# Performance work log

Measured on AMD Instinct MI355X. Metric: run time of the kernel, lower is better.

Reference implementation:

```python
import jax, jax.numpy as jnp
import numpy as np

S, H, A = 8192, 4096, 1024

def setup_inputs() -> dict:
    key = jax.random.key(0)
    ks = jax.random.split(key, 8)
    return {
        "encoder_outputs": jax.random.normal(ks[0], (S, H), jnp.float32),
        "hidden": jax.random.normal(ks[1], (H,), jnp.float32),
        "U_w": jax.random.normal(ks[2], (A, H), jnp.float32) * (1.0 / np.sqrt(H)),
        "U_b": jax.random.normal(ks[3], (A,), jnp.float32) * 0.01,
        "W_w": jax.random.normal(ks[4], (A, H), jnp.float32) * (1.0 / np.sqrt(H)),
        "W_b": jax.random.normal(ks[5], (A,), jnp.float32) * 0.01,
        "V_w": jax.random.normal(ks[6], (1, A), jnp.float32) * (1.0 / np.sqrt(A)),
        "V_b": jax.random.normal(ks[7], (1,), jnp.float32) * 0.01,
    }

def reference(encoder_outputs, hidden, U_w, U_b, W_w, W_b, V_w, V_b):
    # Bahdanau additive attention ('add' mode).
    W_hidden = hidden @ W_w.T + W_b                      # [A]
    U_encode = encoder_outputs @ U_w.T + U_b             # [S, A]
    poly_tanh = jnp.tanh(U_encode + W_hidden)            # [S, A]
    scores = poly_tanh @ V_w.T + V_b                     # [S, 1]
    attn = jax.nn.softmax(scores, axis=0)                # softmax over sequence
    context = attn.T @ encoder_outputs                   # [1, H]
    return context[None]                                 # [1, 1, H] (matches torch bmm)
```

## Files before the change

kernel.cpp:

```cpp
#include <hip/hip_runtime.h>

typedef __attribute__((ext_vector_type(8))) short short8;
typedef __attribute__((ext_vector_type(4))) float f32x4;

#define S_DIM 8192
#define H_DIM 4096
#define A_DIM 1024

__device__ __forceinline__ short f2bf(float x) {
  unsigned u = __float_as_uint(x);
  u += 0x7fffu + ((u >> 16) & 1u);
  return (short)(u >> 16);
}

__device__ __forceinline__ float bf2f(short b) {
  return __uint_as_float(((unsigned)(unsigned short)b) << 16);
}

__device__ __forceinline__ void gload16(const void* g, void* l) {
  __builtin_amdgcn_global_load_lds(
      (const __attribute__((address_space(1))) void*)g,
      (__attribute__((address_space(3))) void*)l, 16, 0, 0);
}

__global__ __launch_bounds__(256) void comb_kernel(const float* __restrict__ hidden,
                                                   const float* __restrict__ Ww,
                                                   const float* __restrict__ Wb,
                                                   const float* __restrict__ Ub,
                                                   float* __restrict__ comb) {
  const int wave = threadIdx.x >> 6;
  const int lane = threadIdx.x & 63;
  const int a = blockIdx.x * 4 + wave;
  const float* row = Ww + (size_t)a * H_DIM;
  float acc = 0.f;
  for (int k = lane * 4; k < H_DIM; k += 64 * 4) {
    float4 w = *(const float4*)(row + k);
    float4 h = *(const float4*)(hidden + k);
    acc += w.x * h.x + w.y * h.y + w.z * h.z + w.w * h.w;
  }
  #pragma unroll
  for (int mk = 1; mk < 64; mk <<= 1) acc += __shfl_xor(acc, mk);
  if (lane == 0) comb[a] = acc + Wb[a] + Ub[a];
}

__global__ __launch_bounds__(256) void cvt_kernel(const float* __restrict__ src,
                                                  unsigned short* __restrict__ dst,
                                                  int n8) {
  const int stride = gridDim.x * blockDim.x;
  for (int i = blockIdx.x * blockDim.x + threadIdx.x; i < n8; i += stride) {
    float4 a = ((const float4*)src)[(size_t)i * 2];
    float4 b = ((const float4*)src)[(size_t)i * 2 + 1];
    short8 o;
    o[0] = f2bf(a.x); o[1] = f2bf(a.y); o[2] = f2bf(a.z); o[3] = f2bf(a.w);
    o[4] = f2bf(b.x); o[5] = f2bf(b.y); o[6] = f2bf(b.z); o[7] = f2bf(b.w);
    ((short8*)dst)[i] = o;
  }
}

__global__ __launch_bounds__(256) void gemm_score_t64_kernel(
    const unsigned short* __restrict__ A,
    const unsigned short* __restrict__ B,
    const float* __restrict__ comb,
    const float* __restrict__ Vw,
    float* __restrict__ scores) {
  __shared__ __align__(16) unsigned short sA[128 * 64];
  __shared__ __align__(16) unsigned short sB[64 * 64];

  const int tid  = threadIdx.x;
  const int lane = tid & 63;
  const int wave = tid >> 6;
  const int wm = wave >> 1, wn = wave & 1;
  const int m0 = blockIdx.x * 128;
  const int n0 = blockIdx.y * 64;

  const int scol  = (lane & 7) * 8;
  const unsigned short* ga = A + (size_t)(m0 + wave * 32 + (lane >> 3)) * H_DIM + scol;
  const unsigned short* gb = B + (size_t)(n0 + wave * 16 + (lane >> 3)) * H_DIM + scol;

  #define STAGE(kt) do {                                                     \
    const unsigned short* pa_ = ga + (size_t)(kt) * 64;                      \
    const unsigned short* pb_ = gb + (size_t)(kt) * 64;                      \
    _Pragma("unroll")                                                        \
    for (int i_ = 0; i_ < 4; ++i_)                                           \
      gload16(pa_ + (size_t)i_ * 8 * H_DIM, &sA[(wave * 4 + i_) * 512]);     \
    _Pragma("unroll")                                                        \
    for (int i_ = 0; i_ < 2; ++i_)                                           \
      gload16(pb_ + (size_t)i_ * 8 * H_DIM, &sB[(wave * 2 + i_) * 512]);     \
  } while (0)

  f32x4 acc[4][2];
  const f32x4 zero = {0.f, 0.f, 0.f, 0.f};
  #pragma unroll
  for (int i = 0; i < 4; ++i)
    #pragma unroll
    for (int j = 0; j < 2; ++j) acc[i][j] = zero;

  STAGE(0);

  const int NK = H_DIM / 64;
  for (int kt = 0; kt < NK; ++kt) {
    __syncthreads();

    short8 af[2][4], bfr[2][2];
    #pragma unroll
    for (int ks = 0; ks < 2; ++ks) {
      #pragma unroll
      for (int i = 0; i < 4; ++i)
        af[ks][i] = *(const short8*)&sA[(wm * 64 + i * 16 + (lane & 15)) * 64 + ks * 32 + (lane >> 4) * 8];
      #pragma unroll
      for (int j = 0; j < 2; ++j)
        bfr[ks][j] = *(const short8*)&sB[(wn * 32 + j * 16 + (lane & 15)) * 64 + ks * 32 + (lane >> 4) * 8];
    }
    __syncthreads();

    if (kt + 1 < NK) STAGE(kt + 1);

    #pragma unroll
    for (int ks = 0; ks < 2; ++ks)
      #pragma unroll
      for (int i = 0; i < 4; ++i)
        #pragma unroll
        for (int j = 0; j < 2; ++j)
          acc[i][j] = __builtin_amdgcn_mfma_f32_16x16x32_bf16(af[ks][i], bfr[ks][j], acc[i][j], 0, 0, 0);
  }
  #undef STAGE

  float vwv[2], cbv[2];
  #pragma unroll
  for (int j = 0; j < 2; ++j) {
    const int col = n0 + wn * 32 + j * 16 + (lane & 15);
    vwv[j] = Vw[col];
    cbv[j] = comb[col];
  }
  #pragma unroll
  for (int i = 0; i < 4; ++i) {
    #pragma unroll
    for (int r = 0; r < 4; ++r) {
      float s = vwv[0] * tanhf(acc[i][0][r] + cbv[0])
              + vwv[1] * tanhf(acc[i][1][r] + cbv[1]);
      s += __shfl_xor(s, 1);
      s += __shfl_xor(s, 2);
      s += __shfl_xor(s, 4);
      s += __shfl_xor(s, 8);
      if ((lane & 15) == 0) {
        const int grow = m0 + wm * 64 + i * 16 + (lane >> 4) * 4 + r;
        atomicAdd(&scores[grow], s);
      }
    }
  }
}

__global__ __launch_bounds__(1024) void softmax_kernel(const float* __restrict__ scores,
                                                       float* __restrict__ attn) {
  __shared__ float redm[16];
  __shared__ float reds[16];
  const int tid = threadIdx.x;
  const int lane = tid & 63, wid = tid >> 6;
  float v[8];
  float m = -3.0e38f;
  #pragma unroll
  for (int i = 0; i < 8; ++i) { v[i] = scores[i * 1024 + tid]; m = fmaxf(m, v[i]); }
  #pragma unroll
  for (int mk = 1; mk < 64; mk <<= 1) m = fmaxf(m, __shfl_xor(m, mk));
  if (lane == 0) redm[wid] = m;
  __syncthreads();
  float M = redm[0];
  #pragma unroll
  for (int j = 1; j < 16; ++j) M = fmaxf(M, redm[j]);
  float e[8]; float s = 0.f;
  #pragma unroll
  for (int i = 0; i < 8; ++i) { e[i] = __expf(v[i] - M); s += e[i]; }
  #pragma unroll
  for (int mk = 1; mk < 64; mk <<= 1) s += __shfl_xor(s, mk);
  if (lane == 0) reds[wid] = s;
  __syncthreads();
  float T = 0.f;
  #pragma unroll
  for (int j = 0; j < 16; ++j) T += reds[j];
  const float inv = 1.f / T;
  #pragma unroll
  for (int i = 0; i < 8; ++i) attn[i * 1024 + tid] = e[i] * inv;
}

__global__ __launch_bounds__(256) void context_bf_kernel(const unsigned short* __restrict__ Ebf,
                                                         const float* __restrict__ attn,
                                                         float* __restrict__ partial) {
  const int h0 = (blockIdx.x * 256 + threadIdx.x) * 8;
  const int s0 = blockIdx.y * 64;
  float acc[8] = {0.f, 0.f, 0.f, 0.f, 0.f, 0.f, 0.f, 0.f};
  for (int s = s0; s < s0 + 64; ++s) {
    const float w = attn[s];
    short8 e = *(const short8*)(Ebf + (size_t)s * H_DIM + h0);
    #pragma unroll
    for (int j = 0; j < 8; ++j) acc[j] += w * bf2f(e[j]);
  }
  float* p = partial + (size_t)blockIdx.y * H_DIM + h0;
  #pragma unroll
  for (int j = 0; j < 8; ++j) p[j] = acc[j];
}

__global__ __launch_bounds__(256) void context_reduce_kernel(const float* __restrict__ partial,
                                                             float* __restrict__ out) {
  const int h = blockIdx.x * 256 + threadIdx.x;
  float acc = 0.f;
  #pragma unroll 8
  for (int y = 0; y < 128; ++y) acc += partial[(size_t)y * H_DIM + h];
  out[h] = acc;
}


#define LDSW 40
__global__ __launch_bounds__(256) void gemm_score_kernel(const float* __restrict__ E,
                                                         const float* __restrict__ Uw,
                                                         const float* __restrict__ comb,
                                                         const float* __restrict__ Vw,
                                                         float* __restrict__ scores) {
  __shared__ __align__(16) short sA[128 * LDSW];
  __shared__ __align__(16) short sB[128 * LDSW];
  const int tid  = threadIdx.x;
  const int lane = tid & 63;
  const int wave = tid >> 6;
  const int wm = wave >> 1, wn = wave & 1;
  const int m0 = blockIdx.x * 128;
  const int n0 = blockIdx.y * 128;
  const int sr = tid >> 1;
  const int sh = tid & 1;
  const float* gA = E  + (size_t)(m0 + sr) * H_DIM + sh * 16;
  const float* gB = Uw + (size_t)(n0 + sr) * H_DIM + sh * 16;
  alignas(16) float fa[16], fb[16];
  #pragma unroll
  for (int j = 0; j < 4; ++j) {
    *(float4*)&fa[j * 4] = *(const float4*)(gA + j * 4);
    *(float4*)&fb[j * 4] = *(const float4*)(gB + j * 4);
  }
  f32x4 acc[4][4];
  const f32x4 zero = {0.f, 0.f, 0.f, 0.f};
  #pragma unroll
  for (int i = 0; i < 4; ++i)
    #pragma unroll
    for (int j = 0; j < 4; ++j) acc[i][j] = zero;
  short* wA = &sA[sr * LDSW + sh * 16];
  short* wB = &sB[sr * LDSW + sh * 16];
  const int NK = H_DIM / 32;
  for (int kt = 0; kt < NK; ++kt) {
    short8 ca0, ca1, cb0, cb1;
    #pragma unroll
    for (int j = 0; j < 8; ++j) {
      ca0[j] = f2bf(fa[j]);     ca1[j] = f2bf(fa[8 + j]);
      cb0[j] = f2bf(fb[j]);     cb1[j] = f2bf(fb[8 + j]);
    }
    __syncthreads();
    *(short8*)(wA)     = ca0;
    *(short8*)(wA + 8) = ca1;
    *(short8*)(wB)     = cb0;
    *(short8*)(wB + 8) = cb1;
    __syncthreads();
    if (kt + 1 < NK) {
      const float* pA = gA + (kt + 1) * 32;
      const float* pB = gB + (kt + 1) * 32;
      #pragma unroll
      for (int j = 0; j < 4; ++j) {
        *(float4*)&fa[j * 4] = *(const float4*)(pA + j * 4);
        *(float4*)&fb[j * 4] = *(const float4*)(pB + j * 4);
      }
    }
    short8 af[4], bfr[4];
    #pragma unroll
    for (int i = 0; i < 4; ++i)
      af[i] = *(const short8*)&sA[(wm * 64 + i * 16 + (lane & 15)) * LDSW + (lane >> 4) * 8];
    #pragma unroll
    for (int j = 0; j < 4; ++j)
      bfr[j] = *(const short8*)&sB[(wn * 64 + j * 16 + (lane & 15)) * LDSW + (lane >> 4) * 8];
    #pragma unroll
    for (int i = 0; i < 4; ++i)
      #pragma unroll
      for (int j = 0; j < 4; ++j)
        acc[i][j] = __builtin_amdgcn_mfma_f32_16x16x32_bf16(af[i], bfr[j], acc[i][j], 0, 0, 0);
  }
  float vwv[4], cbv[4];
  #pragma unroll
  for (int j = 0; j < 4; ++j) {
    const int col = n0 + wn * 64 + j * 16 + (lane & 15);
    vwv[j] = Vw[col];
    cbv[j] = comb[col];
  }
  #pragma unroll
  for (int i = 0; i < 4; ++i) {
    #pragma unroll
    for (int r = 0; r < 4; ++r) {
      float s = 0.f;
      #pragma unroll
      for (int j = 0; j < 4; ++j)
        s += vwv[j] * tanhf(acc[i][j][r] + cbv[j]);
      s += __shfl_xor(s, 1);
      s += __shfl_xor(s, 2);
      s += __shfl_xor(s, 4);
      s += __shfl_xor(s, 8);
      if ((lane & 15) == 0) {
        const int grow = m0 + wm * 64 + i * 16 + (lane >> 4) * 4 + r;
        atomicAdd(&scores[grow], s);
      }
    }
  }
}

__global__ __launch_bounds__(256) void context_kernel(const float* __restrict__ E,
                                                      const float* __restrict__ attn,
                                                      float* __restrict__ out) {
  const int h  = blockIdx.x * 256 + threadIdx.x;
  const int s0 = blockIdx.y * 256;
  float acc = 0.f;
  #pragma unroll 4
  for (int s = s0; s < s0 + 256; ++s)
    acc += attn[s] * E[(size_t)s * H_DIM + h];
  atomicAdd(&out[h], acc);
}


extern "C" void kernel_launch(void* const* d_in, const int* in_sizes, int n_in,
                              void* d_out, int out_size, void* d_ws, size_t ws_size,
                              hipStream_t stream) {
  const float* E   = (const float*)d_in[0];
  const float* hid = (const float*)d_in[1];
  const float* Uw  = (const float*)d_in[2];
  const float* Ub  = (const float*)d_in[3];
  const float* Ww  = (const float*)d_in[4];
  const float* Wb  = (const float*)d_in[5];
  const float* Vw  = (const float*)d_in[6];

  float* out    = (float*)d_out;
  float* ws     = (float*)d_ws;
  float* comb   = ws;
  float* scores = ws + 1024;
  float* attn   = ws + 1024 + 8192;
  float* ctxp   = ws + 17408;
  const size_t CTXP = (size_t)128 * H_DIM;

  unsigned short* Ebf  = (unsigned short*)(ws + 17408 + CTXP);
  unsigned short* Uwbf = Ebf + (size_t)S_DIM * H_DIM;
  const size_t NEED = ((size_t)17408 + CTXP) * 4
                    + ((size_t)S_DIM + A_DIM) * H_DIM * 2;

  hipMemsetAsync(scores, 0, S_DIM * sizeof(float), stream);

  comb_kernel<<<A_DIM / 4, 256, 0, stream>>>(hid, Ww, Wb, Ub, comb);

  if (ws_size >= NEED) {
    cvt_kernel<<<2048, 256, 0, stream>>>(E, Ebf, (int)((size_t)S_DIM * H_DIM / 8));
    cvt_kernel<<<512, 256, 0, stream>>>(Uw, Uwbf, (int)((size_t)A_DIM * H_DIM / 8));

    gemm_score_t64_kernel<<<dim3(S_DIM / 128, A_DIM / 64), 256, 0, stream>>>(
        Ebf, Uwbf, comb, Vw, scores);

    softmax_kernel<<<1, 1024, 0, stream>>>(scores, attn);

    context_bf_kernel<<<dim3(H_DIM / 2048, S_DIM / 64), 256, 0, stream>>>(Ebf, attn, ctxp);
    context_reduce_kernel<<<H_DIM / 256, 256, 0, stream>>>(ctxp, out);
  } else {
    hipMemsetAsync(out, 0, (size_t)out_size * sizeof(float), stream);
    gemm_score_kernel<<<dim3(S_DIM / 128, A_DIM / 128), 256, 0, stream>>>(E, Uw, comb, Vw, scores);
    softmax_kernel<<<1, 1024, 0, stream>>>(scores, attn);
    context_kernel<<<dim3(H_DIM / 256, 32), 256, 0, stream>>>(E, attn, out);
  }
}
```

Baseline: 182.6 us.

## Rework score GEMM with larger 256x128 tiles, triple-buffered LDS and XOR swizzle

Replaces the 128x64 single-buffered score GEMM with a 512-thread kernel using 256x128 block tiles, a 3-stage LDS ring with asynchronous global-to-LDS loads issued two tiles ahead, and one barrier per K step. LDS columns are XOR-swizzled to cut bank conflicts on fragment reads, and setprio is raised around the MFMA bursts. Each wave now computes a 64x64 tile, which doubles register accumulators and raises LDS use to about 144KB per block, so occupancy may be limited.

```diff
diff --git a/kernel.cpp b/kernel.cpp
--- a/kernel.cpp
+++ b/kernel.cpp
@@ -57,78 +57,92 @@
   }
 }
 
-__global__ __launch_bounds__(256) void gemm_score_t64_kernel(
+__global__ __launch_bounds__(512, 2) void gemm_score_8p_kernel(
     const unsigned short* __restrict__ A,
     const unsigned short* __restrict__ B,
     const float* __restrict__ comb,
     const float* __restrict__ Vw,
     float* __restrict__ scores) {
-  __shared__ __align__(16) unsigned short sA[128 * 64];
-  __shared__ __align__(16) unsigned short sB[64 * 64];
+  __shared__ __align__(16) unsigned short sA[3][256 * 64];
+  __shared__ __align__(16) unsigned short sB[3][128 * 64];
 
   const int tid  = threadIdx.x;
   const int lane = tid & 63;
   const int wave = tid >> 6;
-  const int wm = wave >> 1, wn = wave & 1;
-  const int m0 = blockIdx.x * 128;
-  const int n0 = blockIdx.y * 64;
-
-  const int scol  = (lane & 7) * 8;
-  const unsigned short* ga = A + (size_t)(m0 + wave * 32 + (lane >> 3)) * H_DIM + scol;
-  const unsigned short* gb = B + (size_t)(n0 + wave * 16 + (lane >> 3)) * H_DIM + scol;
-
-  #define STAGE(kt) do {                                                     \
-    const unsigned short* pa_ = ga + (size_t)(kt) * 64;                      \
-    const unsigned short* pb_ = gb + (size_t)(kt) * 64;                      \
-    _Pragma("unroll")                                                        \
-    for (int i_ = 0; i_ < 4; ++i_)                                           \
-      gload16(pa_ + (size_t)i_ * 8 * H_DIM, &sA[(wave * 4 + i_) * 512]);     \
-    _Pragma("unroll")                                                        \
-    for (int i_ = 0; i_ < 2; ++i_)                                           \
-      gload16(pb_ + (size_t)i_ * 8 * H_DIM, &sB[(wave * 2 + i_) * 512]);     \
+  const int wm = wave >> 1;
+  const int wn = wave & 1;
+  const int m0 = blockIdx.x * 256;
+  const int n0 = blockIdx.y * 128;
+
+  const int permEl = (((lane & 7) ^ (lane >> 3)) * 8);
+  const unsigned short* gA = A + (size_t)(m0 + wave * 32 + (lane >> 3)) * H_DIM + permEl;
+  const unsigned short* gB = B + (size_t)(n0 + wave * 16 + (lane >> 3)) * H_DIM + permEl;
+
+  #define STAGE(kt, bf) do {                                                  \
+    const unsigned short* pa_ = gA + (size_t)(kt) * 64;                       \
+    const unsigned short* pb_ = gB + (size_t)(kt) * 64;                       \
+    _Pragma("unroll")                                                         \
+    for (int l_ = 0; l_ < 4; ++l_)                                            \
+      gload16(pa_ + (size_t)l_ * 8 * H_DIM, &sA[bf][(wave * 4 + l_) * 512]);  \
+    _Pragma("unroll")                                                         \
+    for (int l_ = 0; l_ < 2; ++l_)                                            \
+      gload16(pb_ + (size_t)l_ * 8 * H_DIM, &sB[bf][(wave * 2 + l_) * 512]);  \
   } while (0)
 
-  f32x4 acc[4][2];
+  const int rA  = lane & 15;
+  const int grp = lane >> 4;
+  const int lx  = lane & 7;
+
+  f32x4 acc[4][4];
   const f32x4 zero = {0.f, 0.f, 0.f, 0.f};
   #pragma unroll
   for (int i = 0; i < 4; ++i)
     #pragma unroll
-    for (int j = 0; j < 2; ++j) acc[i][j] = zero;
-
-  STAGE(0);
-
-  const int NK = H_DIM / 64;
-  for (int kt = 0; kt < NK; ++kt) {
-    __syncthreads();
-
-    short8 af[2][4], bfr[2][2];
+    for (int j = 0; j < 4; ++j) acc[i][j] = zero;
+
+  STAGE(0, 0);
+  STAGE(1, 1);
+  asm volatile("s_waitcnt vmcnt(6)");
+  __builtin_amdgcn_s_barrier();
+  __builtin_amdgcn_sched_barrier(0);
+
+  const int NT = H_DIM / 64;
+  for (int t = 0; t < NT; ++t) {
+    const int cur = t % 3;
+    if (t + 2 < NT) STAGE(t + 2, (t + 2) % 3);
+
+    const unsigned short* a_ = sA[cur];
+    const unsigned short* b_ = sB[cur];
     #pragma unroll
     for (int ks = 0; ks < 2; ++ks) {
+      short8 af[4], bfr[4];
       #pragma unroll
       for (int i = 0; i < 4; ++i)
-        af[ks][i] = *(const short8*)&sA[(wm * 64 + i * 16 + (lane & 15)) * 64 + ks * 32 + (lane >> 4) * 8];
-      #pragma unroll
-      for (int j = 0; j < 2; ++j)
-        bfr[ks][j] = *(const short8*)&sB[(wn * 32 + j * 16 + (lane & 15)) * 64 + ks * 32 + (lane >> 4) * 8];
-    }
-    __syncthreads();
-
-    if (kt + 1 < NK) STAGE(kt + 1);
-
-    #pragma unroll
-    for (int ks = 0; ks < 2; ++ks)
+        af[i] = *(const short8*)&a_[(wm * 64 + i * 16 + rA) * 64 + (((ks * 4 + grp) ^ lx) * 8)];
+      #pragma unroll
+      for (int j = 0; j < 4; ++j)
+        bfr[j] = *(const short8*)&b_[(wn * 64 + j * 16 + rA) * 64 + (((ks * 4 + grp) ^ lx) * 8)];
+      __builtin_amdgcn_s_setprio(1);
       #pragma unroll
       for (int i = 0; i < 4; ++i)
         #pragma unroll
-        for (int j = 0; j < 2; ++j)
-          acc[i][j] = __builtin_amdgcn_mfma_f32_16x16x32_bf16(af[ks][i], bfr[ks][j], acc[i][j], 0, 0, 0);
+        for (int j = 0; j < 4; ++j)
+          acc[i][j] = __builtin_amdgcn_mfma_f32_16x16x32_bf16(af[i], bfr[j], acc[i][j], 0, 0, 0);
+      __builtin_amdgcn_s_setprio(0);
+    }
+
+    __builtin_amdgcn_sched_barrier(0);
+    if (t < NT - 2) asm volatile("s_waitcnt vmcnt(6)");
+    else            asm volatile("s_waitcnt vmcnt(0)");
+    __builtin_amdgcn_s_barrier();
+    __builtin_amdgcn_sched_barrier(0);
   }
   #undef STAGE
 
-  float vwv[2], cbv[2];
-  #pragma unroll
-  for (int j = 0; j < 2; ++j) {
-    const int col = n0 + wn * 32 + j * 16 + (lane & 15);
+  float vwv[4], cbv[4];
+  #pragma unroll
+  for (int j = 0; j < 4; ++j) {
+    const int col = n0 + wn * 64 + j * 16 + rA;
     vwv[j] = Vw[col];
     cbv[j] = comb[col];
   }
@@ -136,14 +150,16 @@
   for (int i = 0; i < 4; ++i) {
     #pragma unroll
     for (int r = 0; r < 4; ++r) {
-      float s = vwv[0] * tanhf(acc[i][0][r] + cbv[0])
-              + vwv[1] * tanhf(acc[i][1][r] + cbv[1]);
+      float s = 0.f;
+      #pragma unroll
+      for (int j = 0; j < 4; ++j)
+        s += vwv[j] * tanhf(acc[i][j][r] + cbv[j]);
       s += __shfl_xor(s, 1);
       s += __shfl_xor(s, 2);
       s += __shfl_xor(s, 4);
       s += __shfl_xor(s, 8);
-      if ((lane & 15) == 0) {
-        const int grow = m0 + wm * 64 + i * 16 + (lane >> 4) * 4 + r;
+      if (rA == 0) {
+        const int grow = m0 + wm * 64 + i * 16 + grp * 4 + r;
         atomicAdd(&scores[grow], s);
       }
     }
@@ -349,7 +365,7 @@
     cvt_kernel<<<2048, 256, 0, stream>>>(E, Ebf, (int)((size_t)S_DIM * H_DIM / 8));
     cvt_kernel<<<512, 256, 0, stream>>>(Uw, Uwbf, (int)((size_t)A_DIM * H_DIM / 8));
 
-    gemm_score_t64_kernel<<<dim3(S_DIM / 128, A_DIM / 64), 256, 0, stream>>>(
+    gemm_score_8p_kernel<<<dim3(S_DIM / 256, A_DIM / 128), 512, 0, stream>>>(
         Ebf, Uwbf, comb, Vw, scores);
 
     softmax_kernel<<<1, 1024, 0, stream>>>(scores, attn);
```

After: 164.2 us. -10.0%, faster.

## Use two-wave 64x64 per-wave tiles in score GEMM and fast tanh

Applied to the files above, without the earlier changes.

Restructures the score GEMM from four waves each computing a 64x32 sub-tile to two waves each computing a 64x64 sub-tile of the same 128x64 block tile. Each wave reads all of the B tile from shared memory and issues more global-to-LDS loads per stage. The aim is more MFMA work per LDS fragment load. It also swaps tanhf for an exp-and-divide approximation in the epilogue. The trade-off is fewer waves per block and more accumulator registers per wave, which may reduce latency hiding, plus slightly lower tanh accuracy.

```diff
diff --git a/kernel.cpp b/kernel.cpp
--- a/kernel.cpp
+++ b/kernel.cpp
@@ -15,6 +15,12 @@
 
 __device__ __forceinline__ float bf2f(short b) {
   return __uint_as_float(((unsigned)(unsigned short)b) << 16);
+}
+
+__device__ __forceinline__ float fast_tanh(float x) {
+  float e = __expf(-2.f * fabsf(x));
+  float r = __fdividef(1.f - e, 1.f + e);
+  return copysignf(r, x);
 }
 
 __device__ __forceinline__ void gload16(const void* g, void* l) {
@@ -57,7 +63,7 @@
   }
 }
 
-__global__ __launch_bounds__(256) void gemm_score_t64_kernel(
+__global__ __launch_bounds__(128) void gemm_score_f_kernel(
     const unsigned short* __restrict__ A,
     const unsigned short* __restrict__ B,
     const float* __restrict__ comb,
@@ -69,31 +75,30 @@
   const int tid  = threadIdx.x;
   const int lane = tid & 63;
   const int wave = tid >> 6;
-  const int wm = wave >> 1, wn = wave & 1;
   const int m0 = blockIdx.x * 128;
   const int n0 = blockIdx.y * 64;
 
-  const int scol  = (lane & 7) * 8;
-  const unsigned short* ga = A + (size_t)(m0 + wave * 32 + (lane >> 3)) * H_DIM + scol;
-  const unsigned short* gb = B + (size_t)(n0 + wave * 16 + (lane >> 3)) * H_DIM + scol;
-
-  #define STAGE(kt) do {                                                     \
-    const unsigned short* pa_ = ga + (size_t)(kt) * 64;                      \
-    const unsigned short* pb_ = gb + (size_t)(kt) * 64;                      \
-    _Pragma("unroll")                                                        \
-    for (int i_ = 0; i_ < 4; ++i_)                                           \
-      gload16(pa_ + (size_t)i_ * 8 * H_DIM, &sA[(wave * 4 + i_) * 512]);     \
-    _Pragma("unroll")                                                        \
-    for (int i_ = 0; i_ < 2; ++i_)                                           \
-      gload16(pb_ + (size_t)i_ * 8 * H_DIM, &sB[(wave * 2 + i_) * 512]);     \
+  const int scol = (lane & 7) * 8;
+  const unsigned short* ga = A + (size_t)(m0 + wave * 64 + (lane >> 3)) * H_DIM + scol;
+  const unsigned short* gb = B + (size_t)(n0 + wave * 32 + (lane >> 3)) * H_DIM + scol;
+
+  #define STAGE(kt) do {                                                      \
+    const unsigned short* pa_ = ga + (size_t)(kt) * 64;                       \
+    const unsigned short* pb_ = gb + (size_t)(kt) * 64;                       \
+    _Pragma("unroll")                                                         \
+    for (int i_ = 0; i_ < 8; ++i_)                                            \
+      gload16(pa_ + (size_t)i_ * 8 * H_DIM, &sA[(wave * 64 + i_ * 8) * 64]);  \
+    _Pragma("unroll")                                                         \
+    for (int i_ = 0; i_ < 4; ++i_)                                            \
+      gload16(pb_ + (size_t)i_ * 8 * H_DIM, &sB[(wave * 32 + i_ * 8) * 64]);  \
   } while (0)
 
-  f32x4 acc[4][2];
+  f32x4 acc[4][4];
   const f32x4 zero = {0.f, 0.f, 0.f, 0.f};
   #pragma unroll
   for (int i = 0; i < 4; ++i)
     #pragma unroll
-    for (int j = 0; j < 2; ++j) acc[i][j] = zero;
+    for (int j = 0; j < 4; ++j) acc[i][j] = zero;
 
   STAGE(0);
 
@@ -101,15 +106,15 @@
   for (int kt = 0; kt < NK; ++kt) {
     __syncthreads();
 
-    short8 af[2][4], bfr[2][2];
+    short8 af[2][4], bfr[2][4];
     #pragma unroll
     for (int ks = 0; ks < 2; ++ks) {
       #pragma unroll
       for (int i = 0; i < 4; ++i)
-        af[ks][i] = *(const short8*)&sA[(wm * 64 + i * 16 + (lane & 15)) * 64 + ks * 32 + (lane >> 4) * 8];
-      #pragma unroll
-      for (int j = 0; j < 2; ++j)
-        bfr[ks][j] = *(const short8*)&sB[(wn * 32 + j * 16 + (lane & 15)) * 64 + ks * 32 + (lane >> 4) * 8];
+        af[ks][i] = *(const short8*)&sA[(wave * 64 + i * 16 + (lane & 15)) * 64 + ks * 32 + (lane >> 4) * 8];
+      #pragma unroll
+      for (int j = 0; j < 4; ++j)
+        bfr[ks][j] = *(const short8*)&sB[(j * 16 + (lane & 15)) * 64 + ks * 32 + (lane >> 4) * 8];
     }
     __syncthreads();
 
@@ -120,15 +125,15 @@
       #pragma unroll
       for (int i = 0; i < 4; ++i)
         #pragma unroll
-        for (int j = 0; j < 2; ++j)
+        for (int j = 0; j < 4; ++j)
           acc[i][j] = __builtin_amdgcn_mfma_f32_16x16x32_bf16(af[ks][i], bfr[ks][j], acc[i][j], 0, 0, 0);
   }
   #undef STAGE
 
-  float vwv[2], cbv[2];
-  #pragma unroll
-  for (int j = 0; j < 2; ++j) {
-    const int col = n0 + wn * 32 + j * 16 + (lane & 15);
+  float vwv[4], cbv[4];
+  #pragma unroll
+  for (int j = 0; j < 4; ++j) {
+    const int col = n0 + j * 16 + (lane & 15);
     vwv[j] = Vw[col];
     cbv[j] = comb[col];
   }
@@ -136,14 +141,16 @@
   for (int i = 0; i < 4; ++i) {
     #pragma unroll
     for (int r = 0; r < 4; ++r) {
-      float s = vwv[0] * tanhf(acc[i][0][r] + cbv[0])
-              + vwv[1] * tanhf(acc[i][1][r] + cbv[1]);
+      float s = 0.f;
+      #pragma unroll
+      for (int j = 0; j < 4; ++j)
+        s += vwv[j] * fast_tanh(acc[i][j][r] + cbv[j]);
       s += __shfl_xor(s, 1);
       s += __shfl_xor(s, 2);
       s += __shfl_xor(s, 4);
       s += __shfl_xor(s, 8);
       if ((lane & 15) == 0) {
-        const int grow = m0 + wm * 64 + i * 16 + (lane >> 4) * 4 + r;
+        const int grow = m0 + wave * 64 + i * 16 + (lane >> 4) * 4 + r;
         atomicAdd(&scores[grow], s);
       }
     }
@@ -291,7 +298,7 @@
       float s = 0.f;
       #pragma unroll
       for (int j = 0; j < 4; ++j)
-        s += vwv[j] * tanhf(acc[i][j][r] + cbv[j]);
+        s += vwv[j] * fast_tanh(acc[i][j][r] + cbv[j]);
       s += __shfl_xor(s, 1);
       s += __shfl_xor(s, 2);
       s += __shfl_xor(s, 4);
@@ -332,7 +339,7 @@
   float* ws     = (float*)d_ws;
   float* comb   = ws;
   float* scores = ws + 1024;
-  float* attn   = ws + 1024 + 8192;
+  float* attn   = ws + 9216;
   float* ctxp   = ws + 17408;
   const size_t CTXP = (size_t)128 * H_DIM;
 
@@ -349,7 +356,7 @@
     cvt_kernel<<<2048, 256, 0, stream>>>(E, Ebf, (int)((size_t)S_DIM * H_DIM / 8));
     cvt_kernel<<<512, 256, 0, stream>>>(Uw, Uwbf, (int)((size_t)A_DIM * H_DIM / 8));
 
-    gemm_score_t64_kernel<<<dim3(S_DIM / 128, A_DIM / 64), 256, 0, stream>>>(
+    gemm_score_f_kernel<<<dim3(S_DIM / 128, A_DIM / 64), 128, 0, stream>>>(
         Ebf, Uwbf, comb, Vw, scores);
 
     softmax_kernel<<<1, 1024, 0, stream>>>(scores, attn);
```

Measured after the change: 176.9 us. -3.1%, faster.
